# Kernel tuning notes

Measured on AMD Instinct MI355X. Metric: run time of the kernel, lower is better.

## Reference

```python
import jax, jax.numpy as jnp
import numpy as np

B, C, H, W = 4, 384, 128, 128
HEADS = 8
D = C // HEADS  # per-head channels
EPS = 1e-5


def _dwconv3x3(y, w, b):
    # y: (B,C,H,W), w: (C,1,3,3) depthwise, b: (C,)
    out = jax.lax.conv_general_dilated(
        y, w, window_strides=(1, 1), padding='SAME',
        dimension_numbers=('NCHW', 'OIHW', 'NCHW'),
        feature_group_count=y.shape[1])
    return out + b[None, :, None, None]


def _proj(xn, wp, bp, wd, bd):
    # convBlock: 1x1 pointwise conv then 3x3 depthwise conv
    y = jnp.einsum('bchw,oc->bohw', xn, wp) + bp[None, :, None, None]
    return _dwconv3x3(y, wd, bd)


def setup_inputs() -> dict:
    key = jax.random.key(0)
    ks = jax.random.split(key, 12)
    s = 0.02
    inp = {
        'x': jax.random.normal(ks[0], (B, C, H, W), dtype=jnp.float32),
        'ln_gamma': jnp.ones((C,), jnp.float32),
        'ln_beta': jnp.zeros((C,), jnp.float32),
        'wq_p': jax.random.normal(ks[1], (C, C), jnp.float32) * s,
        'bq_p': jnp.zeros((C,), jnp.float32),
        'wq_d': jax.random.normal(ks[2], (C, 1, 3, 3), jnp.float32) * s,
        'bq_d': jnp.zeros((C,), jnp.float32),
        'wk_p': jax.random.normal(ks[3], (C, C), jnp.float32) * s,
        'bk_p': jnp.zeros((C,), jnp.float32),
        'wk_d': jax.random.normal(ks[4], (C, 1, 3, 3), jnp.float32) * s,
        'bk_d': jnp.zeros((C,), jnp.float32),
        'wv_p': jax.random.normal(ks[5], (C, C), jnp.float32) * s,
        'bv_p': jnp.zeros((C,), jnp.float32),
        'wv_d': jax.random.normal(ks[6], (C, 1, 3, 3), jnp.float32) * s,
        'bv_d': jnp.zeros((C,), jnp.float32),
        'alpha': jnp.ones((HEADS,), jnp.float32),
        'wf': jax.random.normal(ks[7], (C, C), jnp.float32) * s,
        'bf': jnp.zeros((C,), jnp.float32),
    }
    return inp


def reference(x, ln_gamma, ln_beta,
              wq_p, bq_p, wq_d, bq_d,
              wk_p, bk_p, wk_d, bk_d,
              wv_p, bv_p, wv_d, bv_d,
              alpha, wf, bf):
    # LayerNorm over channel dim (applied per pixel)
    mu = jnp.mean(x, axis=1, keepdims=True)
    var = jnp.var(x, axis=1, keepdims=True)
    xn = (x - mu) * jax.lax.rsqrt(var + EPS)
    xn = xn * ln_gamma[None, :, None, None] + ln_beta[None, :, None, None]

    # QKV projections for all heads at once (heads stacked along out-channels)
    Q = _proj(xn, wq_p, bq_p, wq_d, bq_d).reshape(B, HEADS, D, H, W)
    K = _proj(xn, wk_p, bk_p, wk_d, bk_d).reshape(B, HEADS, D, H, W)
    V = _proj(xn, wv_p, bv_p, wv_d, bv_d).reshape(B, HEADS, D, H, W)

    # channel attention: scores[b,n,i,j] = sum_{hw} K[b,n,i]*Q[b,n,j] / alpha[n]
    scores = jnp.einsum('bnihw,bnjhw->bnij', K, Q) / alpha[None, :, None, None]
    soft = jax.nn.softmax(scores, axis=-1)  # (B,HEADS,D,D)
    # O[b,n,j,h,w] = sum_i V[b,n,i,h,w] * soft[b,n,i,j]
    out = jnp.einsum('bnihw,bnij->bnjhw', V, soft).reshape(B, C, H, W)

    # final 1x1 conv + residual (residual is the layer-normed x, matching the torch code)
    x_cap = jnp.einsum('bchw,oc->bohw', out, wf) + bf[None, :, None, None] + xn
    return x_cap
```

## Files before the change

### kernel.cpp

```cpp
#include <hip/hip_runtime.h>

#define HW    16384
#define WD    128
#define CCH   384
#define NB    4
#define NHEAD 8
#define DH    48
#define NCHUNK 16

typedef unsigned short u16;
typedef unsigned int   u32;
typedef __bf16 bf16x8 __attribute__((ext_vector_type(8)));
typedef float  f32x4  __attribute__((ext_vector_type(4)));

__device__ __forceinline__ float bf2f(u16 u){ u32 t=((u32)u)<<16; float f; __builtin_memcpy(&f,&t,4); return f; }
__device__ __forceinline__ u16 f2bf(float f){ u32 x; __builtin_memcpy(&x,&f,4); u32 r=x+0x7fffu+((x>>16)&1u); return (u16)(r>>16); }
__device__ __forceinline__ f32x4 zero4(){ f32x4 z = {0.f,0.f,0.f,0.f}; return z; }

#define GL16(g,l) __builtin_amdgcn_global_load_lds(\
    (const __attribute__((address_space(1))) void*)(g), \
    (__attribute__((address_space(3))) void*)(l), 16, 0, 0)

__global__ void prep_kernel(const float* wq_p, const float* wk_p, const float* wv_p,
                            const float* bq_p, const float* bk_p, const float* bv_p,
                            const float* wq_d, const float* wk_d, const float* wv_d,
                            const float* bq_d, const float* bk_d, const float* bv_d,
                            u16* Wqkv, float* bias_p, float* wdc, float* bdc)
{
    int idx = blockIdx.x*256 + threadIdx.x;
    const int NW = 3*CCH*CCH;
    if (idx < NW) {
        int m = idx / CCH, c = idx % CCH;
        int w = m / CCH, o = m % CCH;
        const float* src = (w==0)? wq_p : (w==1)? wk_p : wv_p;
        Wqkv[idx] = f2bf(src[o*CCH + c]);
    } else if (idx < NW + 3*CCH) {
        int m = idx - NW; int w = m/CCH, o = m%CCH;
        const float* src = (w==0)? bq_p : (w==1)? bk_p : bv_p;
        bias_p[m] = src[o];
    } else if (idx < NW + 3*CCH + 3*CCH*9) {
        int r = idx - NW - 3*CCH; int m = r/9, k = r%9;
        int w = m/CCH, o = m%CCH;
        const float* src = (w==0)? wq_d : (w==1)? wk_d : wv_d;
        wdc[r] = src[o*9 + k];
    } else if (idx < NW + 3*CCH + 3*CCH*9 + 3*CCH) {
        int m = idx - NW - 3*CCH - 3*CCH*9; int w = m/CCH, o = m%CCH;
        const float* src = (w==0)? bq_d : (w==1)? bk_d : bv_d;
        bdc[m] = src[o];
    }
}

__global__ __launch_bounds__(512, 4) void ln_kernel(
    const float* __restrict__ x, const float* __restrict__ gamma,
    const float* __restrict__ beta, u16* __restrict__ xnt)
{
    __shared__ __align__(16) char lds[32*392*2 + 512];
    u16  (*tile)[392] = (u16(*)[392])lds;
    f32x4* redS  = (f32x4*)lds;
    f32x4* redS2 = (f32x4*)(lds + 8192);
    float* mu_s  = (float*)(lds + 32*392*2);
    float* rs_s  = mu_s + 64;
    int b  = blockIdx.y;
    int p0 = blockIdx.x*64;
    int t  = threadIdx.x;
    int tx = t & 15, cg = t >> 4;
    const float* xb = x + (size_t)b*CCH*HW + p0 + tx*4;
    f32x4 vals[12];
    f32x4 s = zero4(), s2 = zero4();
    #pragma unroll
    for (int cc = 0; cc < 12; ++cc) {
        f32x4 v = *(const f32x4*)(xb + (size_t)(cg*12+cc)*HW);
        vals[cc] = v;
        s += v; s2 += v*v;
    }
    redS[cg*16+tx] = s; redS2[cg*16+tx] = s2;
    __syncthreads();
    if (t < 64) {
        int q = t >> 2, comp = t & 3;
        const float* rs1 = (const float*)redS;
        const float* rs2 = (const float*)redS2;
        float st = 0.f, st2 = 0.f;
        #pragma unroll
        for (int g2 = 0; g2 < 32; ++g2) {
            st  += rs1[(g2*16+q)*4 + comp];
            st2 += rs2[(g2*16+q)*4 + comp];
        }
        float mu  = st*(1.f/CCH);
        float var = st2*(1.f/CCH) - mu*mu;
        mu_s[t] = mu;
        rs_s[t] = rsqrtf(var + 1e-5f);
    }
    __syncthreads();
    f32x4 mu4, rs4;
    #pragma unroll
    for (int j = 0; j < 4; ++j) { mu4[j] = mu_s[tx*4+j]; rs4[j] = rs_s[tx*4+j]; }
    u32 pk[12][2];
    #pragma unroll
    for (int cc = 0; cc < 12; ++cc) {
        int c = cg*12 + cc;
        float gm = gamma[c], bt = beta[c];
        f32x4 v = (vals[cc] - mu4) * rs4;
        u16 o0 = f2bf(v[0]*gm + bt), o1 = f2bf(v[1]*gm + bt);
        u16 o2 = f2bf(v[2]*gm + bt), o3 = f2bf(v[3]*gm + bt);
        pk[cc][0] = (u32)o0 | ((u32)o1 << 16);
        pk[cc][1] = (u32)o2 | ((u32)o3 << 16);
    }
    u16* xto = xnt + (size_t)b*CCH*HW;
    int half = tx >> 3, txl = tx & 7;
    #pragma unroll
    for (int p2 = 0; p2 < 2; ++p2) {
        if (half == p2) {
            #pragma unroll
            for (int i = 0; i < 4; ++i) {
                int row = txl*4 + i;
                #pragma unroll
                for (int j = 0; j < 3; ++j) {
                    #define EXTB(cc) ((pk[cc][i>>1] >> (16*(i&1))) & 0xffffu)
                    u32 a0 = EXTB(4*j+0) | (EXTB(4*j+1) << 16);
                    u32 a1 = EXTB(4*j+2) | (EXTB(4*j+3) << 16);
                    #undef EXTB
                    uint2 pr; pr.x = a0; pr.y = a1;
                    *(uint2*)&tile[row][cg*12 + j*4] = pr;
                }
            }
        }
        __syncthreads();
        #pragma unroll
        for (int k = 0; k < 3; ++k) {
            int idx = t + k*512;
            int p = idx / 48, q = idx % 48;
            *(uint4*)(xto + (size_t)(p0 + p2*32 + p)*CCH + q*8) = *(const uint4*)&tile[p][q*8];
        }
        __syncthreads();
    }
}

template<int EPI, int TRANSB>
__global__ __launch_bounds__(512) void gemm_nt(
    const u16* __restrict__ A, const u16* __restrict__ Bm, void* __restrict__ Cout,
    const float* __restrict__ bias, const u16* __restrict__ xnadd,
    long A_bstride, long B_bstride, long C_bstride)
{
    constexpr int SMBYTES = TRANSB ? 65536 : 32768;
    __shared__ __align__(16) char smraw[SMBYTES];
    u16* smA = (u16*)smraw;
    u16* smB = (u16*)(smraw + (TRANSB ? 32768 : 16384));

    int gx = gridDim.x, gy = gridDim.y;
    int Ngrid = gx*gy*gridDim.z;
    int lin = blockIdx.x + gx*(blockIdx.y + gy*blockIdx.z);
    int swz = ((Ngrid & 7) == 0) ? ((lin & 7)*(Ngrid >> 3) + (lin >> 3)) : lin;
    int bx = swz % gx; int rem = swz / gx;
    int by = rem % gy; int b  = rem / gy;
    int m0 = bx*128, n0 = by*128;

    const u16* Ab = A  + (size_t)b*A_bstride;
    const u16* Bb = Bm + (size_t)b*B_bstride;
    int t = threadIdx.x;
    int lane = t & 63, w = t >> 6;
    int wr = w >> 2, wc = w & 3;
    int l15 = lane & 15, g = lane >> 4;
    int s7 = l15 & 7;

    int rowA[2], kksA[2];
    #pragma unroll
    for (int r = 0; r < 2; ++r) {
        int e = (r*512 + t)*8;
        rowA[r] = e >> 6;
        int kk  = e & 63;
        kksA[r] = kk ^ ((rowA[r]&7)<<3);
    }
    int cB  = (2*t) & 63;
    int pxg = (2*t) >> 6;

    f32x4 acc[4][2];
    #pragma unroll
    for (int i=0;i<4;++i) { acc[i][0] = zero4(); acc[i][1] = zero4(); }

#define COMPUTE(sAp, sBp) { \
    const u16* sA_ = (sAp); const u16* sB_ = (sBp); \
    _Pragma("unroll") \
    for (int kh = 0; kh < 2; ++kh) { \
        int u = (kh*4 + g) ^ s7; \
        bf16x8 af[4], bq[2]; \
        _Pragma("unroll") \
        for (int mi=0;mi<4;++mi) { \
            int row = wr*64 + mi*16 + l15; \
            af[mi] = *(const bf16x8*)&sA_[row*64 + u*8]; \
        } \
        _Pragma("unroll") \
        for (int nj=0;nj<2;++nj) { \
            int row = wc*32 + nj*16 + l15; \
            bq[nj] = *(const bf16x8*)&sB_[row*64 + u*8]; \
        } \
        _Pragma("unroll") \
        for (int mi=0;mi<4;++mi) \
            _Pragma("unroll") \
            for (int nj=0;nj<2;++nj) \
                acc[mi][nj] = __builtin_amdgcn_mfma_f32_16x16x32_bf16(af[mi], bq[nj], acc[mi][nj], 0,0,0); \
    } }

#define WRITE_SMB(dst, va, vb) { \
    u16 e0[8], e1[8]; \
    __builtin_memcpy(e0,&(va),16); __builtin_memcpy(e1,&(vb),16); \
    _Pragma("unroll") \
    for (int j=0;j<8;++j) { \
        u32 wv = (u32)e0[j] | ((u32)e1[j]<<16); \
        *(u32*)((dst) + (pxg*8+j)*64 + (cB ^ (j<<3))) = wv; \
    } }

    if (!TRANSB) {
        #pragma unroll
        for (int r = 0; r < 2; ++r) {
            GL16(Ab + (size_t)(m0+rowA[r])*CCH + kksA[r], smA + r*4096 + w*512);
            GL16(Bb + (size_t)(n0+rowA[r])*CCH + kksA[r], smB + r*4096 + w*512);
        }
        __syncthreads();
        for (int ks = 0; ks < 6; ++ks) {
            COMPUTE(smA, smB);
            if (ks < 5) {
                __syncthreads();
                int k1 = (ks+1)*64;
                #pragma unroll
                for (int r = 0; r < 2; ++r) {
                    GL16(Ab + (size_t)(m0+rowA[r])*CCH + k1 + kksA[r], smA + r*4096 + w*512);
                    GL16(Bb + (size_t)(n0+rowA[r])*CCH + k1 + kksA[r], smB + r*4096 + w*512);
                }
                __syncthreads();
            }
        }
    } else {
        uint4 s0a, s0b, s1a, s1b;
        s0a = *(const uint4*)(Bb + (size_t)cB*HW     + n0 + pxg*8);
        s0b = *(const uint4*)(Bb + (size_t)(cB+1)*HW + n0 + pxg*8);
        #pragma unroll
        for (int r = 0; r < 2; ++r)
            GL16(Ab + (size_t)(m0+rowA[r])*CCH + kksA[r], smA + r*4096 + w*512);
        WRITE_SMB(smB, s0a, s0b);
        s1a = *(const uint4*)(Bb + (size_t)(64+cB)*HW   + n0 + pxg*8);
        s1b = *(const uint4*)(Bb + (size_t)(64+cB+1)*HW + n0 + pxg*8);
        asm volatile("s_waitcnt vmcnt(2)" ::: "memory");
        asm volatile("s_waitcnt lgkmcnt(0)" ::: "memory");
        __builtin_amdgcn_sched_barrier(0);
        __builtin_amdgcn_s_barrier();

        #pragma unroll
        for (int ks = 0; ks < 6; ++ks) {
            int cur = ks & 1, nxt = cur ^ 1;
            if (ks < 5) {
                int k1 = (ks+1)*64;
                #pragma unroll
                for (int r = 0; r < 2; ++r)
                    GL16(Ab + (size_t)(m0+rowA[r])*CCH + k1 + kksA[r],
                         smA + nxt*8192 + r*4096 + w*512);
            }
            if (ks < 4) {
                int k2 = (ks+2)*64;
                if ((ks & 1) == 0) {
                    s0a = *(const uint4*)(Bb + (size_t)(k2+cB)*HW   + n0 + pxg*8);
                    s0b = *(const uint4*)(Bb + (size_t)(k2+cB+1)*HW + n0 + pxg*8);
                } else {
                    s1a = *(const uint4*)(Bb + (size_t)(k2+cB)*HW   + n0 + pxg*8);
                    s1b = *(const uint4*)(Bb + (size_t)(k2+cB+1)*HW + n0 + pxg*8);
                }
            }
            COMPUTE(smA + cur*8192, smB + cur*8192);
            if (ks < 5) {
                if (((ks+1) & 1) == 0) { WRITE_SMB(smB + nxt*8192, s0a, s0b); }
                else                   { WRITE_SMB(smB + nxt*8192, s1a, s1b); }
                if (ks < 4) asm volatile("s_waitcnt vmcnt(2)" ::: "memory");
                else        asm volatile("s_waitcnt vmcnt(0)" ::: "memory");
                asm volatile("s_waitcnt lgkmcnt(0)" ::: "memory");
                __builtin_amdgcn_sched_barrier(0);
                __builtin_amdgcn_s_barrier();
            }
        }
    }

    if (EPI == 0) {
        #pragma unroll
        for (int mi=0;mi<4;++mi) {
            #pragma unroll
            for (int r=0;r<4;++r) {
                int grow = m0 + wr*64 + mi*16 + g*4 + r;
                float bv = bias[grow];
                #pragma unroll
                for (int nj=0;nj<2;++nj) {
                    int gcol = n0 + wc*32 + nj*16 + l15;
                    ((u16*)Cout)[(size_t)b*C_bstride + (size_t)grow*HW + gcol] = f2bf(acc[mi][nj][r] + bv);
                }
            }
        }
    } else {
        float* epi = (float*)smraw;
        u16*   xt  = (u16*)(smraw + 33792);
        const u16* xtg = xnadd + (size_t)b*CCH*HW;
        #pragma unroll
        for (int half = 0; half < 2; ++half) {
            __syncthreads();
            #pragma unroll
            for (int q2 = 0; q2 < 2; ++q2) {
                int idx2 = t*2 + q2;
                int px  = idx2 >> 3;
                int oct = idx2 & 7;
                int chl = (oct < 4) ? (half*32 + oct*8) : (64 + half*32 + (oct-4)*8);
                uint4 v4 = *(const uint4*)(xtg + (size_t)(n0+px)*CCH + m0 + chl);
                u16 e[8]; __builtin_memcpy(e, &v4, 16);
                int col = oct*8;
                #pragma unroll
                for (int j = 0; j < 8; ++j)
                    xt[(col+j)*132 + px] = e[j];
            }
            #pragma unroll
            for (int mi2 = 0; mi2 < 2; ++mi2) {
                int mi = half*2 + mi2;
                #pragma unroll
                for (int r = 0; r < 4; ++r) {
                    int lrow = wr*32 + mi2*16 + g*4 + r;
                    int grow = m0 + wr*64 + half*32 + mi2*16 + g*4 + r;
                    float bv = bias[grow];
                    #pragma unroll
                    for (int nj = 0; nj < 2; ++nj)
                        epi[lrow*132 + wc*32 + nj*16 + l15] = acc[mi][nj][r] + bv;
                }
            }
            __syncthreads();
            #pragma unroll
            for (int k = 0; k < 4; ++k) {
                int idx = t + k*512;
                int lrow = idx >> 5, cq = idx & 31;
                int grow = m0 + (lrow>>5)*64 + half*32 + (lrow&31);
                int gcol = n0 + cq*4;
                f32x4 v = *(const f32x4*)&epi[lrow*132 + cq*4];
                uint2 xv = *(const uint2*)&xt[lrow*132 + cq*4];
                v[0] += bf2f((u16)xv.x);        v[1] += bf2f((u16)(xv.x>>16));
                v[2] += bf2f((u16)xv.y);        v[3] += bf2f((u16)(xv.y>>16));
                *(f32x4*)((float*)Cout + (size_t)b*C_bstride + (size_t)grow*HW + gcol) = v;
            }
        }
    }
#undef COMPUTE
#undef WRITE_SMB
}

__global__ __launch_bounds__(256) void dw_kernel(
    const u16* __restrict__ in, u16* __restrict__ out,
    const float* __restrict__ wd, const float* __restrict__ bd, int cpb)
{
    __shared__ __align__(16) u16 srow[20*WD];
    int b  = blockIdx.z;
    int c  = blockIdx.y;
    int yt = blockIdx.x;
    int t  = threadIdx.x;
    int lane = t & 63, w = t >> 6;
    int y0 = yt*16;
    const u16* plane = in + (size_t)b*cpb*HW + (size_t)c*HW;
    {
        int r  = t >> 4;
        int sg = t & 15;
        int yy = y0 - 1 + r;
        yy = yy < 0 ? 0 : (yy >= WD ? WD-1 : yy);
        GL16(plane + (size_t)yy*WD + sg*8, srow + w*4*WD);
    }
    if (t < 64) {
        int r  = 16 + (t >> 4);
        int sg = t & 15;
        int yy = y0 - 1 + r;
        yy = yy < 0 ? 0 : (yy >= WD ? WD-1 : yy);
        GL16(plane + (size_t)yy*WD + sg*8, srow + 16*WD);
    }
    __syncthreads();
    if (yt == 0 && t < 16)
        ((uint4*)srow)[t] = make_uint4(0,0,0,0);
    if (yt == (WD/16 - 1) && t < 16)
        *((uint4*)(srow + 17*WD) + t) = make_uint4(0,0,0,0);
    __syncthreads();

    int ty = t >> 4, tx = t & 15;
    int y  = y0 + ty;
    int x0 = tx*8;
    float w9[9];
    #pragma unroll
    for (int i=0;i<9;++i) w9[i] = wd[c*9+i];
    float bv = bd[c];
    float rows[3][10];
    #pragma unroll
    for (int dy=0; dy<3; ++dy) {
        const u16* rp = srow + (ty+dy)*WD;
        rows[dy][0] = (tx==0) ? 0.f : bf2f(rp[x0-1]);
        uint4 v = *(const uint4*)(rp + x0);
        u16 e[8]; __builtin_memcpy(e,&v,16);
        #pragma unroll
        for (int i=0;i<8;++i) rows[dy][1+i] = bf2f(e[i]);
        rows[dy][9] = (tx==15) ? 0.f : bf2f(rp[x0+8]);
    }
    u16 ovals[8];
    #pragma unroll
    for (int xo=0; xo<8; ++xo) {
        float a = bv;
        #pragma unroll
        for (int dy=0;dy<3;++dy)
            #pragma unroll
            for (int dx=0;dx<3;++dx)
                a += rows[dy][xo+dx] * w9[dy*3+dx];
        ovals[xo] = f2bf(a);
    }
    uint4 ov; __builtin_memcpy(&ov, ovals, 16);
    *(uint4*)(out + (size_t)b*cpb*HW + (size_t)c*HW + y*WD + x0) = ov;
}

__global__ void scores_kernel(const u16* __restrict__ Kp, const u16* __restrict__ Qp,
                              float* __restrict__ S_part, int cpb)
{
    int pc = blockIdx.x;
    int h  = blockIdx.y;
    int b  = blockIdx.z;
    int lane = threadIdx.x;
    int l15 = lane & 15, g = lane >> 4;
    const u16* Kb = Kp + (size_t)b*cpb*HW + (size_t)(h*DH)*HW;
    const u16* Qb = Qp + (size_t)b*cpb*HW + (size_t)(h*DH)*HW;
    int p0 = pc*(HW/NCHUNK);
    f32x4 acc[3][3];
    #pragma unroll
    for (int i=0;i<3;++i)
        #pragma unroll
        for (int j=0;j<3;++j) acc[i][j] = zero4();
    for (int kk=0; kk<(HW/NCHUNK)/32; ++kk) {
        int p = p0 + kk*32 + g*8;
        bf16x8 af[3], bq[3];
        #pragma unroll
        for (int it=0; it<3; ++it)
            af[it] = *(const bf16x8*)(Kb + (size_t)(it*16 + l15)*HW + p);
        #pragma unroll
        for (int jt=0; jt<3; ++jt)
            bq[jt] = *(const bf16x8*)(Qb + (size_t)(jt*16 + l15)*HW + p);
        #pragma unroll
        for (int it=0;it<3;++it)
            #pragma unroll
            for (int jt=0;jt<3;++jt)
                acc[it][jt] = __builtin_amdgcn_mfma_f32_16x16x32_bf16(af[it], bq[jt], acc[it][jt], 0,0,0);
    }
    float* Sp = S_part + ((size_t)pc*32 + b*NHEAD + h)*(DH*DH);
    #pragma unroll
    for (int it=0;it<3;++it)
        #pragma unroll
        for (int jt=0;jt<3;++jt)
            #pragma unroll
            for (int r=0;r<4;++r) {
                int i = it*16 + g*4 + r;
                int j = jt*16 + l15;
                Sp[i*DH + j] = acc[it][jt][r];
            }
}

__global__ void sm_kernel(const float* __restrict__ S_part, const float* __restrict__ alpha,
                          float* __restrict__ soft)
{
    __shared__ float S[DH*DH];
    int bh = blockIdx.x;
    int h  = bh & 7;
    int t  = threadIdx.x;
    float ia = 1.f / alpha[h];
    for (int e = t; e < DH*DH; e += 256) {
        float s = 0.f;
        #pragma unroll
        for (int pc=0; pc<NCHUNK; ++pc) s += S_part[((size_t)pc*32 + bh)*(DH*DH) + e];
        S[e] = s * ia;
    }
    __syncthreads();
    if (t < DH) {
        float m = -1e30f;
        for (int j=0;j<DH;++j) m = fmaxf(m, S[t*DH+j]);
        float sum = 0.f;
        for (int j=0;j<DH;++j) sum += __expf(S[t*DH+j]-m);
        float inv = 1.f/sum;
        for (int j=0;j<DH;++j)
            soft[(size_t)bh*(DH*DH) + t*DH + j] = __expf(S[t*DH+j]-m)*inv;
    }
}

__global__ __launch_bounds__(256) void fold_kernel(const float* __restrict__ wf,
                                                   const float* __restrict__ soft,
                                                   u16* __restrict__ wf_eff)
{
    __shared__ float softl[DH*DH];
    __shared__ float wfl[16*DH];
    int ob = blockIdx.x, h = blockIdx.y, b = blockIdx.z;
    int t = threadIdx.x;
    const float* sb = soft + ((size_t)(b*NHEAD + h))*(DH*DH);
    for (int k = t; k < DH*DH; k += 256) softl[k] = sb[k];
    for (int k = t; k < 16*DH; k += 256) {
        int ol = k / DH, j = k % DH;
        wfl[k] = wf[(size_t)(ob*16 + ol)*CCH + h*DH + j];
    }
    __syncthreads();
    #pragma unroll
    for (int r = 0; r < 3; ++r) {
        int out = r*256 + t;
        int ol = out / DH, i = out % DH;
        const f32x4* wr_ = (const f32x4*)&wfl[ol*DH];
        const f32x4* sr  = (const f32x4*)&softl[i*DH];
        f32x4 a4 = zero4();
        #pragma unroll
        for (int j = 0; j < 12; ++j) a4 += wr_[j]*sr[j];
        float a = a4[0]+a4[1]+a4[2]+a4[3];
        wf_eff[((size_t)b*CCH + ob*16 + ol)*CCH + h*DH + i] = f2bf(a);
    }
}

extern "C" void kernel_launch(void* const* d_in, const int* in_sizes, int n_in,
                              void* d_out, int out_size, void* d_ws, size_t ws_size,
                              hipStream_t stream)
{
    const float* x    = (const float*)d_in[0];
    const float* ln_g = (const float*)d_in[1];
    const float* ln_b = (const float*)d_in[2];
    const float* wq_p = (const float*)d_in[3];
    const float* bq_p = (const float*)d_in[4];
    const float* wq_d = (const float*)d_in[5];
    const float* bq_d = (const float*)d_in[6];
    const float* wk_p = (const float*)d_in[7];
    const float* bk_p = (const float*)d_in[8];
    const float* wk_d = (const float*)d_in[9];
    const float* bk_d = (const float*)d_in[10];
    const float* wv_p = (const float*)d_in[11];
    const float* bv_p = (const float*)d_in[12];
    const float* wv_d = (const float*)d_in[13];
    const float* bv_d = (const float*)d_in[14];
    const float* alpha= (const float*)d_in[15];
    const float* wf   = (const float*)d_in[16];
    const float* bf_  = (const float*)d_in[17];

    char* ws = (char*)d_ws;
    size_t off = 0;
    auto alloc = [&](size_t bytes)->char* { char* p = ws + off; off += (bytes + 255) & ~(size_t)255; return p; };
    const size_t BIG  = (size_t)NB*CCH*HW*2;
    const size_t BIG3 = 3*BIG;
    const size_t SMALLS = (size_t)3*CCH*CCH*2 + 3*CCH*4 + 3*CCH*9*4 + 3*CCH*4
                        + (size_t)NCHUNK*32*DH*DH*4 + (size_t)32*DH*DH*4
                        + (size_t)NB*CCH*CCH*2 + 16*256;
    const size_t NEED_FUSED = BIG + 2*BIG3 + SMALLS;
    const bool fused = (ws_size >= NEED_FUSED);
    const long BStr = (long)CCH*HW;

    if (fused) {
        u16* xn_t   = (u16*)alloc(BIG);
        u16* pwQKV  = (u16*)alloc(BIG3);
        u16* dwQKV  = (u16*)alloc(BIG3);
        u16*   Wqkv   = (u16*)  alloc((size_t)3*CCH*CCH*2);
        float* bias_p = (float*)alloc((size_t)3*CCH*4);
        float* wdc    = (float*)alloc((size_t)3*CCH*9*4);
        float* bdc    = (float*)alloc((size_t)3*CCH*4);
        float* S_part = (float*)alloc((size_t)NCHUNK*32*DH*DH*4);
        float* soft   = (float*)alloc((size_t)32*DH*DH*4);
        u16*   wf_eff = (u16*)  alloc((size_t)NB*CCH*CCH*2);

        prep_kernel<<<1778, 256, 0, stream>>>(wq_p,wk_p,wv_p, bq_p,bk_p,bv_p,
                                              wq_d,wk_d,wv_d, bq_d,bk_d,bv_d,
                                              Wqkv, bias_p, wdc, bdc);
        ln_kernel<<<dim3(256,NB), 512, 0, stream>>>(x, ln_g, ln_b, xn_t);
        gemm_nt<0,0><<<dim3(9,128,NB), 512, 0, stream>>>(Wqkv, xn_t, pwQKV, bias_p, nullptr,
                                                         0, BStr, (long)3*CCH*HW);
        dw_kernel<<<dim3(8,3*CCH,NB), 256, 0, stream>>>(pwQKV, dwQKV, wdc, bdc, 3*CCH);
        scores_kernel<<<dim3(NCHUNK,NHEAD,NB), 64, 0, stream>>>(dwQKV + (size_t)CCH*HW,
                                                                dwQKV,
                                                                S_part, 3*CCH);
        sm_kernel<<<32, 256, 0, stream>>>(S_part, alpha, soft);
        fold_kernel<<<dim3(CCH/16, NHEAD, NB), 256, 0, stream>>>(wf, soft, wf_eff);
        gemm_nt<1,1><<<dim3(3,128,NB), 512, 0, stream>>>(wf_eff, dwQKV + (size_t)2*CCH*HW,
                                                         d_out, bf_, xn_t,
                                                         (long)CCH*CCH, (long)3*CCH*HW, BStr);
    } else {
        u16* xn_t  = (u16*)alloc(BIG);
        u16* pwA   = (u16*)alloc(BIG);
        u16* dwQ   = (u16*)alloc(BIG);
        u16* dwK   = (u16*)alloc(BIG);
        u16*   Wqkv   = (u16*)  alloc((size_t)3*CCH*CCH*2);
        float* bias_p = (float*)alloc((size_t)3*CCH*4);
        float* wdc    = (float*)alloc((size_t)3*CCH*9*4);
        float* bdc    = (float*)alloc((size_t)3*CCH*4);
        float* S_part = (float*)alloc((size_t)NCHUNK*32*DH*DH*4);
        float* soft   = (float*)alloc((size_t)32*DH*DH*4);
        u16*   wf_eff = (u16*)  alloc((size_t)NB*CCH*CCH*2);
        if (off > ws_size) return;
        u16* dwV = dwQ;

        prep_kernel<<<1778, 256, 0, stream>>>(wq_p,wk_p,wv_p, bq_p,bk_p,bv_p,
                                              wq_d,wk_d,wv_d, bq_d,bk_d,bv_d,
                                              Wqkv, bias_p, wdc, bdc);
        ln_kernel<<<dim3(256,NB), 512, 0, stream>>>(x, ln_g, ln_b, xn_t);
        gemm_nt<0,0><<<dim3(3,128,NB), 512, 0, stream>>>(Wqkv,           xn_t, pwA, bias_p,       nullptr, 0, BStr, BStr);
        dw_kernel<<<dim3(8,CCH,NB), 256, 0, stream>>>(pwA, dwQ, wdc,         bdc,       CCH);
        gemm_nt<0,0><<<dim3(3,128,NB), 512, 0, stream>>>(Wqkv + CCH*CCH, xn_t, pwA, bias_p + CCH, nullptr, 0, BStr, BStr);
        dw_kernel<<<dim3(8,CCH,NB), 256, 0, stream>>>(pwA, dwK, wdc + CCH*9, bdc + CCH, CCH);
        scores_kernel<<<dim3(NCHUNK,NHEAD,NB), 64, 0, stream>>>(dwK, dwQ, S_part, CCH);
        sm_kernel<<<32, 256, 0, stream>>>(S_part, alpha, soft);
        fold_kernel<<<dim3(CCH/16, NHEAD, NB), 256, 0, stream>>>(wf, soft, wf_eff);
        gemm_nt<0,0><<<dim3(3,128,NB), 512, 0, stream>>>(Wqkv + 2*CCH*CCH, xn_t, pwA, bias_p + 2*CCH, nullptr, 0, BStr, BStr);
        dw_kernel<<<dim3(8,CCH,NB), 256, 0, stream>>>(pwA, dwV, wdc + 2*CCH*9, bdc + 2*CCH, CCH);
        gemm_nt<1,1><<<dim3(3,128,NB), 512, 0, stream>>>(wf_eff, dwV, d_out, bf_, xn_t,
                                                         (long)CCH*CCH, BStr, BStr);
    }
}
```

Before: 282.5 us.

## Fuse prep into LN launch, softmax into fold, and split scores across warps

Merges the weight-prep kernel into the layernorm launch as extra blocks, removes the separate softmax kernel by having each fold block reduce partial scores and compute the softmax itself, and widens the scores kernel to four waves per block with an LDS reduction. The aim is fewer kernel launches and more parallelism in the latency-bound scores stage. In exchange, every fold block redundantly re-reduces all score partials and recomputes the softmax, and the prep grid now spans all batch rows, with idle blocks returning early.

```diff
diff --git a/kernel.cpp b/kernel.cpp
--- a/kernel.cpp
+++ b/kernel.cpp
@@ -7,6 +7,7 @@
 #define NHEAD 8
 #define DH    48
 #define NCHUNK 16
+#define PREPB 889
 
 typedef unsigned short u16;
 typedef unsigned int   u32;
@@ -21,39 +22,40 @@
     (const __attribute__((address_space(1))) void*)(g), \
     (__attribute__((address_space(3))) void*)(l), 16, 0, 0)
 
-__global__ void prep_kernel(const float* wq_p, const float* wk_p, const float* wv_p,
-                            const float* bq_p, const float* bk_p, const float* bv_p,
-                            const float* wq_d, const float* wk_d, const float* wv_d,
-                            const float* bq_d, const float* bk_d, const float* bv_d,
-                            u16* Wqkv, float* bias_p, float* wdc, float* bdc)
+__global__ __launch_bounds__(512, 4) void ln_prep_kernel(
+    const float* __restrict__ x, const float* __restrict__ gamma,
+    const float* __restrict__ beta, u16* __restrict__ xnt,
+    const float* wq_p, const float* wk_p, const float* wv_p,
+    const float* bq_p, const float* bk_p, const float* bv_p,
+    const float* wq_d, const float* wk_d, const float* wv_d,
+    const float* bq_d, const float* bk_d, const float* bv_d,
+    u16* Wqkv, float* bias_p, float* wdc, float* bdc)
 {
-    int idx = blockIdx.x*256 + threadIdx.x;
-    const int NW = 3*CCH*CCH;
-    if (idx < NW) {
-        int m = idx / CCH, c = idx % CCH;
-        int w = m / CCH, o = m % CCH;
-        const float* src = (w==0)? wq_p : (w==1)? wk_p : wv_p;
-        Wqkv[idx] = f2bf(src[o*CCH + c]);
-    } else if (idx < NW + 3*CCH) {
-        int m = idx - NW; int w = m/CCH, o = m%CCH;
-        const float* src = (w==0)? bq_p : (w==1)? bk_p : bv_p;
-        bias_p[m] = src[o];
-    } else if (idx < NW + 3*CCH + 3*CCH*9) {
-        int r = idx - NW - 3*CCH; int m = r/9, k = r%9;
-        int w = m/CCH, o = m%CCH;
-        const float* src = (w==0)? wq_d : (w==1)? wk_d : wv_d;
-        wdc[r] = src[o*9 + k];
-    } else if (idx < NW + 3*CCH + 3*CCH*9 + 3*CCH) {
-        int m = idx - NW - 3*CCH - 3*CCH*9; int w = m/CCH, o = m%CCH;
-        const float* src = (w==0)? bq_d : (w==1)? bk_d : bv_d;
-        bdc[m] = src[o];
-    }
-}
-
-__global__ __launch_bounds__(512, 4) void ln_kernel(
-    const float* __restrict__ x, const float* __restrict__ gamma,
-    const float* __restrict__ beta, u16* __restrict__ xnt)
-{
+    if (blockIdx.x >= 256) {
+        if (blockIdx.y != 0) return;
+        int idx = (blockIdx.x - 256)*512 + threadIdx.x;
+        const int NW = 3*CCH*CCH;
+        if (idx < NW) {
+            int m = idx / CCH, c = idx % CCH;
+            int w = m / CCH, o = m % CCH;
+            const float* src = (w==0)? wq_p : (w==1)? wk_p : wv_p;
+            Wqkv[idx] = f2bf(src[o*CCH + c]);
+        } else if (idx < NW + 3*CCH) {
+            int m = idx - NW; int w = m/CCH, o = m%CCH;
+            const float* src = (w==0)? bq_p : (w==1)? bk_p : bv_p;
+            bias_p[m] = src[o];
+        } else if (idx < NW + 3*CCH + 3*CCH*9) {
+            int r = idx - NW - 3*CCH; int m = r/9, k = r%9;
+            int w = m/CCH, o = m%CCH;
+            const float* src = (w==0)? wq_d : (w==1)? wk_d : wv_d;
+            wdc[r] = src[o*9 + k];
+        } else if (idx < NW + 3*CCH + 3*CCH*9 + 3*CCH) {
+            int m = idx - NW - 3*CCH - 3*CCH*9; int w = m/CCH, o = m%CCH;
+            const float* src = (w==0)? bq_d : (w==1)? bk_d : bv_d;
+            bdc[m] = src[o];
+        }
+        return;
+    }
     __shared__ __align__(16) char lds[32*392*2 + 512];
     u16  (*tile)[392] = (u16(*)[392])lds;
     f32x4* redS  = (f32x4*)lds;
@@ -409,23 +411,27 @@
     *(uint4*)(out + (size_t)b*cpb*HW + (size_t)c*HW + y*WD + x0) = ov;
 }
 
-__global__ void scores_kernel(const u16* __restrict__ Kp, const u16* __restrict__ Qp,
-                              float* __restrict__ S_part, int cpb)
+__global__ __launch_bounds__(256) void scores_kernel(const u16* __restrict__ Kp,
+                                                     const u16* __restrict__ Qp,
+                                                     float* __restrict__ S_part, int cpb)
 {
+    __shared__ float red[3*DH*DH];
     int pc = blockIdx.x;
     int h  = blockIdx.y;
     int b  = blockIdx.z;
-    int lane = threadIdx.x;
+    int t  = threadIdx.x;
+    int lane = t & 63, wv = t >> 6;
     int l15 = lane & 15, g = lane >> 4;
     const u16* Kb = Kp + (size_t)b*cpb*HW + (size_t)(h*DH)*HW;
     const u16* Qb = Qp + (size_t)b*cpb*HW + (size_t)(h*DH)*HW;
-    int p0 = pc*(HW/NCHUNK);
+    int p0 = pc*(HW/NCHUNK) + wv*(HW/NCHUNK/4);
     f32x4 acc[3][3];
     #pragma unroll
     for (int i=0;i<3;++i)
         #pragma unroll
         for (int j=0;j<3;++j) acc[i][j] = zero4();
-    for (int kk=0; kk<(HW/NCHUNK)/32; ++kk) {
+    #pragma unroll
+    for (int kk=0; kk<(HW/NCHUNK/4)/32; ++kk) {
         int p = p0 + kk*32 + g*8;
         bf16x8 af[3], bq[3];
         #pragma unroll
@@ -440,58 +446,68 @@
             for (int jt=0;jt<3;++jt)
                 acc[it][jt] = __builtin_amdgcn_mfma_f32_16x16x32_bf16(af[it], bq[jt], acc[it][jt], 0,0,0);
     }
-    float* Sp = S_part + ((size_t)pc*32 + b*NHEAD + h)*(DH*DH);
-    #pragma unroll
-    for (int it=0;it<3;++it)
-        #pragma unroll
-        for (int jt=0;jt<3;++jt)
-            #pragma unroll
-            for (int r=0;r<4;++r) {
-                int i = it*16 + g*4 + r;
-                int j = jt*16 + l15;
-                Sp[i*DH + j] = acc[it][jt][r];
-            }
+    if (wv > 0) {
+        float* dst = red + (wv-1)*(DH*DH) + lane*36;
+        #pragma unroll
+        for (int it=0;it<3;++it)
+            #pragma unroll
+            for (int jt=0;jt<3;++jt)
+                *(f32x4*)(dst + (it*3+jt)*4) = acc[it][jt];
+    }
+    __syncthreads();
+    if (wv == 0) {
+        #pragma unroll
+        for (int it=0;it<3;++it)
+            #pragma unroll
+            for (int jt=0;jt<3;++jt) {
+                #pragma unroll
+                for (int w2=0; w2<3; ++w2)
+                    acc[it][jt] += *(const f32x4*)(red + w2*(DH*DH) + lane*36 + (it*3+jt)*4);
+            }
+        float* Sp = S_part + ((size_t)pc*32 + b*NHEAD + h)*(DH*DH);
+        #pragma unroll
+        for (int it=0;it<3;++it)
+            #pragma unroll
+            for (int jt=0;jt<3;++jt)
+                #pragma unroll
+                for (int r=0;r<4;++r) {
+                    int i = it*16 + g*4 + r;
+                    int j = jt*16 + l15;
+                    Sp[i*DH + j] = acc[it][jt][r];
+                }
+    }
 }
 
-__global__ void sm_kernel(const float* __restrict__ S_part, const float* __restrict__ alpha,
-                          float* __restrict__ soft)
-{
-    __shared__ float S[DH*DH];
-    int bh = blockIdx.x;
-    int h  = bh & 7;
-    int t  = threadIdx.x;
-    float ia = 1.f / alpha[h];
-    for (int e = t; e < DH*DH; e += 256) {
-        float s = 0.f;
-        #pragma unroll
-        for (int pc=0; pc<NCHUNK; ++pc) s += S_part[((size_t)pc*32 + bh)*(DH*DH) + e];
-        S[e] = s * ia;
-    }
-    __syncthreads();
-    if (t < DH) {
-        float m = -1e30f;
-        for (int j=0;j<DH;++j) m = fmaxf(m, S[t*DH+j]);
-        float sum = 0.f;
-        for (int j=0;j<DH;++j) sum += __expf(S[t*DH+j]-m);
-        float inv = 1.f/sum;
-        for (int j=0;j<DH;++j)
-            soft[(size_t)bh*(DH*DH) + t*DH + j] = __expf(S[t*DH+j]-m)*inv;
-    }
-}
-
 __global__ __launch_bounds__(256) void fold_kernel(const float* __restrict__ wf,
-                                                   const float* __restrict__ soft,
+                                                   const float* __restrict__ S_part,
+                                                   const float* __restrict__ alpha,
                                                    u16* __restrict__ wf_eff)
 {
     __shared__ float softl[DH*DH];
     __shared__ float wfl[16*DH];
     int ob = blockIdx.x, h = blockIdx.y, b = blockIdx.z;
     int t = threadIdx.x;
-    const float* sb = soft + ((size_t)(b*NHEAD + h))*(DH*DH);
-    for (int k = t; k < DH*DH; k += 256) softl[k] = sb[k];
+    int bh = b*NHEAD + h;
+    float ia = 1.f / alpha[h];
+    for (int e = t; e < DH*DH; e += 256) {
+        float s = 0.f;
+        #pragma unroll
+        for (int pc=0; pc<NCHUNK; ++pc) s += S_part[((size_t)pc*32 + bh)*(DH*DH) + e];
+        softl[e] = s * ia;
+    }
     for (int k = t; k < 16*DH; k += 256) {
         int ol = k / DH, j = k % DH;
         wfl[k] = wf[(size_t)(ob*16 + ol)*CCH + h*DH + j];
+    }
+    __syncthreads();
+    if (t < DH) {
+        float m = -1e30f;
+        for (int j=0;j<DH;++j) m = fmaxf(m, softl[t*DH+j]);
+        float sum = 0.f;
+        for (int j=0;j<DH;++j) sum += __expf(softl[t*DH+j]-m);
+        float inv = 1.f/sum;
+        for (int j=0;j<DH;++j)
+            softl[t*DH+j] = __expf(softl[t*DH+j]-m)*inv;
     }
     __syncthreads();
     #pragma unroll
@@ -554,19 +570,19 @@
         float* S_part = (float*)alloc((size_t)NCHUNK*32*DH*DH*4);
         float* soft   = (float*)alloc((size_t)32*DH*DH*4);
         u16*   wf_eff = (u16*)  alloc((size_t)NB*CCH*CCH*2);
-
-        prep_kernel<<<1778, 256, 0, stream>>>(wq_p,wk_p,wv_p, bq_p,bk_p,bv_p,
-                                              wq_d,wk_d,wv_d, bq_d,bk_d,bv_d,
-                                              Wqkv, bias_p, wdc, bdc);
-        ln_kernel<<<dim3(256,NB), 512, 0, stream>>>(x, ln_g, ln_b, xn_t);
+        (void)soft;
+
+        ln_prep_kernel<<<dim3(256+PREPB,NB), 512, 0, stream>>>(
+            x, ln_g, ln_b, xn_t,
+            wq_p,wk_p,wv_p, bq_p,bk_p,bv_p, wq_d,wk_d,wv_d, bq_d,bk_d,bv_d,
+            Wqkv, bias_p, wdc, bdc);
         gemm_nt<0,0><<<dim3(9,128,NB), 512, 0, stream>>>(Wqkv, xn_t, pwQKV, bias_p, nullptr,
                                                          0, BStr, (long)3*CCH*HW);
         dw_kernel<<<dim3(8,3*CCH,NB), 256, 0, stream>>>(pwQKV, dwQKV, wdc, bdc, 3*CCH);
-        scores_kernel<<<dim3(NCHUNK,NHEAD,NB), 64, 0, stream>>>(dwQKV + (size_t)CCH*HW,
-                                                                dwQKV,
-                                                                S_part, 3*CCH);
-        sm_kernel<<<32, 256, 0, stream>>>(S_part, alpha, soft);
-        fold_kernel<<<dim3(CCH/16, NHEAD, NB), 256, 0, stream>>>(wf, soft, wf_eff);
+        scores_kernel<<<dim3(NCHUNK,NHEAD,NB), 256, 0, stream>>>(dwQKV + (size_t)CCH*HW,
+                                                                 dwQKV,
+                                                                 S_part, 3*CCH);
+        fold_kernel<<<dim3(CCH/16, NHEAD, NB), 256, 0, stream>>>(wf, S_part, alpha, wf_eff);
         gemm_nt<1,1><<<dim3(3,128,NB), 512, 0, stream>>>(wf_eff, dwQKV + (size_t)2*CCH*HW,
                                                          d_out, bf_, xn_t,
                                                          (long)CCH*CCH, (long)3*CCH*HW, BStr);
@@ -583,19 +599,19 @@
         float* soft   = (float*)alloc((size_t)32*DH*DH*4);
         u16*   wf_eff = (u16*)  alloc((size_t)NB*CCH*CCH*2);
         if (off > ws_size) return;
+        (void)soft;
         u16* dwV = dwQ;
 
-        prep_kernel<<<1778, 256, 0, stream>>>(wq_p,wk_p,wv_p, bq_p,bk_p,bv_p,
-                                              wq_d,wk_d,wv_d, bq_d,bk_d,bv_d,
-                                              Wqkv, bias_p, wdc, bdc);
-        ln_kernel<<<dim3(256,NB), 512, 0, stream>>>(x, ln_g, ln_b, xn_t);
+        ln_prep_kernel<<<dim3(256+PREPB,NB), 512, 0, stream>>>(
+            x, ln_g, ln_b, xn_t,
+            wq_p,wk_p,wv_p, bq_p,bk_p,bv_p, wq_d,wk_d,wv_d, bq_d,bk_d,bv_d,
+            Wqkv, bias_p, wdc, bdc);
         gemm_nt<0,0><<<dim3(3,128,NB), 512, 0, stream>>>(Wqkv,           xn_t, pwA, bias_p,       nullptr, 0, BStr, BStr);
         dw_kernel<<<dim3(8,CCH,NB), 256, 0, stream>>>(pwA, dwQ, wdc,         bdc,       CCH);
         gemm_nt<0,0><<<dim3(3,128,NB), 512, 0, stream>>>(Wqkv + CCH*CCH, xn_t, pwA, bias_p + CCH, nullptr, 0, BStr, BStr);
         dw_kernel<<<dim3(8,CCH,NB), 256, 0, stream>>>(pwA, dwK, wdc + CCH*9, bdc + CCH, CCH);
-        scores_kernel<<<dim3(NCHUNK,NHEAD,NB), 64, 0, stream>>>(dwK, dwQ, S_part, CCH);
-        sm_kernel<<<32, 256, 0, stream>>>(S_part, alpha, soft);
-        fold_kernel<<<dim3(CCH/16, NHEAD, NB), 256, 0, stream>>>(wf, soft, wf_eff);
+        scores_kernel<<<dim3(NCHUNK,NHEAD,NB), 256, 0, stream>>>(dwK, dwQ, S_part, CCH);
+        fold_kernel<<<dim3(CCH/16, NHEAD, NB), 256, 0, stream>>>(wf, S_part, alpha, wf_eff);
         gemm_nt<0,0><<<dim3(3,128,NB), 512, 0, stream>>>(Wqkv + 2*CCH*CCH, xn_t, pwA, bias_p + 2*CCH, nullptr, 0, BStr, BStr);
         dw_kernel<<<dim3(8,CCH,NB), 256, 0, stream>>>(pwA, dwV, wdc + 2*CCH*9, bdc + 2*CCH, CCH);
         gemm_nt<1,1><<<dim3(3,128,NB), 512, 0, stream>>>(wf_eff, dwV, d_out, bf_, xn_t,
```

Result: faster. 263.1 us, median of 3 (-6.9%).
